# Optimization experiments

Hardware: AMD Instinct MI355X
Metric: run time of the kernel (lower is better)

Reference implementation:

```python
import jax, jax.numpy as jnp
import numpy as np

HID = 1024
BATCH = 32
SRC = 2048

def setup_inputs() -> dict:
    key = jax.random.key(0)
    k1, k2, k3, k4, k5 = jax.random.split(key, 5)
    hidden = jax.random.normal(k1, (BATCH, HID), dtype=jnp.float32)
    encoder_outputs = jax.random.normal(k2, (BATCH, SRC, HID), dtype=jnp.float32)
    # nn.Linear(2H, H): weight [H, 2H], bias [H]
    lim = 1.0 / np.sqrt(2 * HID)
    attn_w = jax.random.uniform(k3, (HID, 2 * HID), dtype=jnp.float32, minval=-lim, maxval=lim)
    attn_b = jax.random.uniform(k4, (HID,), dtype=jnp.float32, minval=-lim, maxval=lim)
    v = jax.random.uniform(k5, (HID,), dtype=jnp.float32)  # torch.rand
    return {"hidden": hidden, "encoder_outputs": encoder_outputs,
            "attn_w": attn_w, "attn_b": attn_b, "v": v}

def reference(hidden, encoder_outputs, attn_w, attn_b, v):
    # Split the concat linear: cat([hidden, enc]) @ W^T == hidden @ Wh^T + enc @ We^T
    w_h = attn_w[:, :HID]          # [H, H] acts on repeated hidden
    w_e = attn_w[:, HID:]          # [H, H] acts on encoder outputs
    # energy: [B, S, H]
    energy = jnp.tanh(
        jnp.einsum('bh,oh->bo', hidden, w_h)[:, None, :]
        + jnp.einsum('bsh,oh->bso', encoder_outputs, w_e)
        + attn_b
    )
    scores = jnp.einsum('bso,o->bs', energy, v)  # [B, S]
    return jax.nn.softmax(scores, axis=1)
```

## Files before the change

kernel.cpp:

```cpp
#include <hip/hip_runtime.h>
#include <hip/hip_bf16.h>

#define HID    1024
#define NBATCH 32
#define SRC    2048
#define MROWS  (NBATCH * SRC)

typedef _Float16 f16;
typedef f16   f16x8 __attribute__((ext_vector_type(8)));
typedef f16   f16x4 __attribute__((ext_vector_type(4)));
typedef float f32x4 __attribute__((ext_vector_type(4)));

#define BAR()    asm volatile("s_barrier" ::: "memory")
#define VMCNT0() asm volatile("s_waitcnt vmcnt(0)" ::: "memory")

__device__ __forceinline__ void gload_lds16(const void* g, void* l) {
  __builtin_amdgcn_global_load_lds(
      (const __attribute__((address_space(1))) void*)g,
      (__attribute__((address_space(3))) void*)l, 16, 0, 0);
}

__device__ __forceinline__ float fast_tanh(float x) {
  x = fminf(fmaxf(x, -15.f), 15.f);
  float e = __expf(2.f * x);
  return (e - 1.f) / (e + 1.f);
}

__global__ void convw_k(const float* __restrict__ attn_w, f16* __restrict__ Wf) {
  int idx = blockIdx.x * 256 + threadIdx.x;
  int j = idx * 4;
  int o = j >> 10, h = j & 1023;
  f32x4 d = *(const f32x4*)(attn_w + (size_t)o * 2048 + HID + h);
  f16x4 q = { (f16)d[0], (f16)d[1], (f16)d[2], (f16)d[3] };
  *(f16x4*)(Wf + (size_t)o * HID + h) = q;
}

__global__ void hvec_k(const float* __restrict__ hidden,
                       const float* __restrict__ attn_w,
                       const float* __restrict__ attn_b,
                       float* __restrict__ hvec) {
  int idx = blockIdx.x * 256 + threadIdx.x;
  int b = idx >> 10, o = idx & 1023;
  const float* wrow = attn_w + (size_t)o * 2048;
  const float* hrow = hidden + (size_t)b * HID;
  float acc = 0.f;
  for (int h = 0; h < HID; h += 4) {
    f32x4 wv = *(const f32x4*)(wrow + h);
    f32x4 hv = *(const f32x4*)(hrow + h);
    acc += wv[0]*hv[0] + wv[1]*hv[1] + wv[2]*hv[2] + wv[3]*hv[3];
  }
  hvec[idx] = acc + attn_b[o];
}

__global__ void convA_k(const float* __restrict__ A, f16* __restrict__ Af) {
  size_t i = ((size_t)blockIdx.x * 256 + threadIdx.x) * 8;
  f32x4 d0 = *(const f32x4*)(A + i);
  f32x4 d1 = *(const f32x4*)(A + i + 4);
  f16x8 q = { (f16)d0[0], (f16)d0[1], (f16)d0[2], (f16)d0[3],
              (f16)d1[0], (f16)d1[1], (f16)d1[2], (f16)d1[3] };
  *(f16x8*)(Af + i) = q;
}


#define STG1(q, Tn, cd) do { \
  const f16* s_ = ((q) < 4 ? Ab : Bb) + \
      (size_t)(((q) & 3) * 64 + (tid >> 3)) * HID + (Tn) * 64 + scol; \
  char* d_ = lds + (cd) * 65536 + ((q) < 4 ? 0 : 32768) + ((q) & 3) * 8192 + w * 1024; \
  gload_lds16(s_, d_); } while (0)

#define PHASE(P, Tn, c, DOSTG) do { \
  const int mh_ = (P) >> 1, nh_ = (P) & 1; \
  const char* la_ = lds + (c) * 65536; \
  const char* lb_ = la_ + 32768; \
  f16x8 aF[4][2], bF[2][2]; \
  _Pragma("unroll") for (int m4 = 0; m4 < 4; ++m4) { \
    const char* rb = la_ + (wr * 128 + mh_ * 64 + m4 * 16 + lr) * 128; \
    aF[m4][0] = *(const f16x8*)(rb + ((lg ^ sw) << 4)); \
    aF[m4][1] = *(const f16x8*)(rb + (((4 + lg) ^ sw) << 4)); \
  } \
  _Pragma("unroll") for (int n2 = 0; n2 < 2; ++n2) { \
    const char* rb = lb_ + (wc * 64 + nh_ * 32 + n2 * 16 + lr) * 128; \
    bF[n2][0] = *(const f16x8*)(rb + ((lg ^ sw) << 4)); \
    bF[n2][1] = *(const f16x8*)(rb + (((4 + lg) ^ sw) << 4)); \
  } \
  if (DOSTG) { STG1(2 * (P), Tn, (c) ^ 1); STG1(2 * (P) + 1, Tn, (c) ^ 1); } \
  BAR(); \
  asm volatile("s_waitcnt lgkmcnt(0)" ::: "memory"); \
  __builtin_amdgcn_sched_barrier(0); \
  __builtin_amdgcn_s_setprio(1); \
  _Pragma("unroll") for (int ks = 0; ks < 2; ++ks) \
  _Pragma("unroll") for (int m4 = 0; m4 < 4; ++m4) \
  _Pragma("unroll") for (int n2 = 0; n2 < 2; ++n2) \
    acc[mh_ * 4 + m4][nh_ * 2 + n2] = __builtin_amdgcn_mfma_f32_16x16x32_f16( \
        aF[m4][ks], bF[n2][ks], acc[mh_ * 4 + m4][nh_ * 2 + n2], 0, 0, 0); \
  __builtin_amdgcn_s_setprio(0); \
  if ((P) == 3 && (DOSTG)) { VMCNT0(); } \
  BAR(); \
} while (0)

__global__ __launch_bounds__(512, 2) void gemm_f16(
    const f16*  __restrict__ Af,
    const f16*  __restrict__ Wf,
    const float* __restrict__ hvec,
    const float* __restrict__ v,
    float* __restrict__ part)
{
  extern __shared__ __align__(16) char lds[];

  int bid = blockIdx.x;
  int wg = (bid & 7) * 128 + (bid >> 3);
  int m_idx = wg >> 2, n_idx = wg & 3;
  long row0 = (long)m_idx * 256;
  int o0 = n_idx * 256;
  int b = (int)(row0 >> 11);

  int tid = threadIdx.x;
  int l = tid & 63, w = tid >> 6;
  int wr = w >> 2, wc = w & 3;
  int lr = l & 15, lg = l >> 4;
  int sw = lr & 7;
  int scol = ((tid & 7) ^ ((tid >> 3) & 7)) * 8;

  const f16* Ab = Af + row0 * HID;
  const f16* Bb = Wf + (size_t)o0 * HID;

  f32x4 acc[8][4];
#pragma unroll
  for (int m = 0; m < 8; ++m)
#pragma unroll
    for (int n = 0; n < 4; ++n) acc[m][n] = (f32x4){0.f, 0.f, 0.f, 0.f};

#pragma unroll
  for (int q = 0; q < 8; ++q) { STG1(q, 0, 0); }
  VMCNT0(); BAR();

#pragma unroll 1
  for (int Tp = 0; Tp < 8; ++Tp) {
    const int Ta = Tp * 2, Tb = Ta + 1;
    PHASE(0, Ta + 1, 0, 1); PHASE(1, Ta + 1, 0, 1);
    PHASE(2, Ta + 1, 0, 1); PHASE(3, Ta + 1, 0, 1);
    const int dob = (Tb < 15);
    PHASE(0, Tb + 1, 1, dob); PHASE(1, Tb + 1, 1, dob);
    PHASE(2, Tb + 1, 1, dob); PHASE(3, Tb + 1, 1, dob);
  }

  float hvv[4], vvv[4];
#pragma unroll
  for (int n = 0; n < 4; ++n) {
    int o = o0 + wc * 64 + n * 16 + lr;
    hvv[n] = hvec[b * HID + o];
    vvv[n] = v[o];
  }
  float* scf = (float*)lds;
  __syncthreads();
#pragma unroll
  for (int m = 0; m < 8; ++m) {
#pragma unroll
    for (int r = 0; r < 4; ++r) {
      float s = 0.f;
#pragma unroll
      for (int n = 0; n < 4; ++n)
        s += fast_tanh(acc[m][n][r] + hvv[n]) * vvv[n];
      s += __shfl_xor(s, 1); s += __shfl_xor(s, 2);
      s += __shfl_xor(s, 4); s += __shfl_xor(s, 8);
      if (lr == 0) scf[wc * 256 + wr * 128 + m * 16 + lg * 4 + r] = s;
    }
  }
  __syncthreads();
  if (tid < 256)
    part[(size_t)n_idx * MROWS + row0 + tid] =
        scf[tid] + scf[256 + tid] + scf[512 + tid] + scf[768 + tid];
}

__global__ __launch_bounds__(256, 2) void gemm_fb(
    const float* __restrict__ A, const f16* __restrict__ Wf,
    const float* __restrict__ hvec, const float* __restrict__ v,
    float* __restrict__ part)
{
  __shared__ __align__(16) f16 lA[128][32];
  __shared__ __align__(16) f16 lB[128][32];
  __shared__ float sc[128];

  int bid = blockIdx.x;
  int x = bid & 7, j = bid >> 3;
  int m_idx = x * 64 + (j >> 3);
  int n_idx = j & 7;
  long row0 = (long)m_idx * 128;
  int o0 = n_idx * 128;
  int b = (int)(row0 >> 11);

  int tid = threadIdx.x;
  int l = tid & 63, w = tid >> 6;
  int wr = w >> 1, wc = w & 1;
  int lr = l & 15, lg = l >> 4;

  f32x4 acc[4][4];
#pragma unroll
  for (int m = 0; m < 4; ++m)
#pragma unroll
    for (int n = 0; n < 4; ++n) acc[m][n] = (f32x4){0.f, 0.f, 0.f, 0.f};

  const float* Abase = A + row0 * 1024;

  for (int k0 = 0; k0 < 1024; k0 += 32) {
    __syncthreads();
#pragma unroll
    for (int i = 0; i < 2; ++i) {
      int rr = (i * 256 + tid) >> 2;
      const f16* src = Wf + (size_t)(o0 + rr) * HID + k0 + (tid & 3) * 8;
      char* ldsb = (char*)&lB[0][0] + i * 4096 + w * 1024;
      gload_lds16(src, ldsb);
    }
#pragma unroll
    for (int i = 0; i < 4; ++i) {
      int ja = i * 256 + tid;
      int arow = ja >> 3, ac4 = ja & 7;
      f32x4 d = *(const f32x4*)(Abase + (size_t)arow * 1024 + k0 + ac4 * 4);
      f16x4 q = { (f16)d[0], (f16)d[1], (f16)d[2], (f16)d[3] };
      *(f16x4*)&lA[arow][ac4 * 4] = q;
    }
    __syncthreads();
    f16x8 aF[4], bF[4];
#pragma unroll
    for (int m = 0; m < 4; ++m)
      aF[m] = *(const f16x8*)&lA[wr * 64 + m * 16 + lr][lg * 8];
#pragma unroll
    for (int n = 0; n < 4; ++n)
      bF[n] = *(const f16x8*)&lB[wc * 64 + n * 16 + lr][lg * 8];
#pragma unroll
    for (int m = 0; m < 4; ++m)
#pragma unroll
      for (int n = 0; n < 4; ++n)
        acc[m][n] = __builtin_amdgcn_mfma_f32_16x16x32_f16(aF[m], bF[n], acc[m][n], 0, 0, 0);
  }

  float hv[4], vv[4];
#pragma unroll
  for (int n = 0; n < 4; ++n) {
    int o = o0 + wc * 64 + n * 16 + lr;
    hv[n] = hvec[b * HID + o];
    vv[n] = v[o];
  }
  float myv[4][4];
#pragma unroll
  for (int m = 0; m < 4; ++m) {
#pragma unroll
    for (int r = 0; r < 4; ++r) {
      float s = 0.f;
#pragma unroll
      for (int n = 0; n < 4; ++n)
        s += fast_tanh(acc[m][n][r] + hv[n]) * vv[n];
      s += __shfl_xor(s, 1); s += __shfl_xor(s, 2);
      s += __shfl_xor(s, 4); s += __shfl_xor(s, 8);
      myv[m][r] = s;
    }
  }
  if (wc == 0 && lr == 0) {
#pragma unroll
    for (int m = 0; m < 4; ++m)
#pragma unroll
      for (int r = 0; r < 4; ++r)
        sc[wr * 64 + m * 16 + lg * 4 + r] = myv[m][r];
  }
  __syncthreads();
  if (wc == 1 && lr == 0) {
#pragma unroll
    for (int m = 0; m < 4; ++m)
#pragma unroll
      for (int r = 0; r < 4; ++r)
        sc[wr * 64 + m * 16 + lg * 4 + r] += myv[m][r];
  }
  __syncthreads();
  if (tid < 128)
    part[(size_t)n_idx * MROWS + row0 + tid] = sc[tid];
}

__global__ void softmax_k(const float* __restrict__ part, float* __restrict__ out,
                          int nsl) {
  int b = blockIdx.x;
  __shared__ float srow[SRC];
  __shared__ float red[8];
  int tid = threadIdx.x;

  float lmax = -1e30f;
  for (int i = tid; i < SRC; i += 256) {
    float s = 0.f;
    for (int t = 0; t < nsl; ++t)
      s += part[(size_t)t * MROWS + (size_t)b * SRC + i];
    srow[i] = s;
    lmax = fmaxf(lmax, s);
  }
#pragma unroll
  for (int off = 32; off >= 1; off >>= 1)
    lmax = fmaxf(lmax, __shfl_xor(lmax, off));
  if ((tid & 63) == 0) red[tid >> 6] = lmax;
  __syncthreads();
  float bmax = fmaxf(fmaxf(red[0], red[1]), fmaxf(red[2], red[3]));

  float lsum = 0.f;
  for (int i = tid; i < SRC; i += 256) {
    float e = __expf(srow[i] - bmax);
    srow[i] = e;
    lsum += e;
  }
#pragma unroll
  for (int off = 32; off >= 1; off >>= 1)
    lsum += __shfl_xor(lsum, off);
  if ((tid & 63) == 0) red[4 + (tid >> 6)] = lsum;
  __syncthreads();
  float inv = 1.f / (red[4] + red[5] + red[6] + red[7]);
  for (int i = tid; i < SRC; i += 256)
    out[(size_t)b * SRC + i] = srow[i] * inv;
}

extern "C" void kernel_launch(void* const* d_in, const int* in_sizes, int n_in,
                              void* d_out, int out_size, void* d_ws, size_t ws_size,
                              hipStream_t stream) {
  const float* hidden = (const float*)d_in[0];
  const float* enc    = (const float*)d_in[1];
  const float* attn_w = (const float*)d_in[2];
  const float* attn_b = (const float*)d_in[3];
  const float* v      = (const float*)d_in[4];
  float* out = (float*)d_out;

  char* ws = (char*)d_ws;
  f16*   Wf   = (f16*)ws;
  float* hv   = (float*)(ws + (2ull << 20));
  float* part = (float*)(ws + (2ull << 20) + (128ull << 10));
  f16*   Af   = (f16*)(ws + (8ull << 20));

  const size_t WS_NEEDED = (8ull << 20) + (128ull << 20);

  convw_k<<<1024, 256, 0, stream>>>(attn_w, Wf);
  hvec_k <<<128,  256, 0, stream>>>(hidden, attn_w, attn_b, hv);

  if (ws_size >= WS_NEEDED) {
    convA_k<<<32768, 256, 0, stream>>>(enc, Af);
    gemm_f16<<<1024, 512, 131072, stream>>>(Af, Wf, hv, v, part);
    softmax_k<<<NBATCH, 256, 0, stream>>>(part, out, 4);
  } else {
    gemm_fb<<<4096, 256, 0, stream>>>(enc, Wf, hv, v, part);
    softmax_k<<<NBATCH, 256, 0, stream>>>(part, out, 8);
  }
}
```

Measured before the change: 300.9 us.

## Reorder GEMM phases to reuse A/B fragments across MFMA quadrants

Restructures each K-tile of the f16 GEMM from four independent phases (each reloading its A and B fragments from LDS) into a snake order that keeps A fragments and two B fragment sets in registers across quadrants. This cuts LDS fragment reads per tile and groups the global-to-LDS stages into one A burst and one B burst. It also replaces the asm barrier with the builtin and drops the memory clobbers, which loosens compiler ordering. The extra live fragment registers could raise register pressure at the 512x2 launch bound.

```diff
diff --git a/kernel.cpp b/kernel.cpp
--- a/kernel.cpp
+++ b/kernel.cpp
@@ -11,8 +11,10 @@
 typedef f16   f16x4 __attribute__((ext_vector_type(4)));
 typedef float f32x4 __attribute__((ext_vector_type(4)));
 
-#define BAR()    asm volatile("s_barrier" ::: "memory")
-#define VMCNT0() asm volatile("s_waitcnt vmcnt(0)" ::: "memory")
+#define BAR()    __builtin_amdgcn_s_barrier()
+#define LGKM0()  asm volatile("s_waitcnt lgkmcnt(0)")
+#define VMCNT0() asm volatile("s_waitcnt vmcnt(0)")
+#define SCHED0() __builtin_amdgcn_sched_barrier(0)
 
 __device__ __forceinline__ void gload_lds16(const void* g, void* l) {
   __builtin_amdgcn_global_load_lds(
@@ -62,40 +64,59 @@
 }
 
 
-#define STG1(q, Tn, cd) do { \
-  const f16* s_ = ((q) < 4 ? Ab : Bb) + \
-      (size_t)(((q) & 3) * 64 + (tid >> 3)) * HID + (Tn) * 64 + scol; \
-  char* d_ = lds + (cd) * 65536 + ((q) < 4 ? 0 : 32768) + ((q) & 3) * 8192 + w * 1024; \
-  gload_lds16(s_, d_); } while (0)
-
-#define PHASE(P, Tn, c, DOSTG) do { \
-  const int mh_ = (P) >> 1, nh_ = (P) & 1; \
-  const char* la_ = lds + (c) * 65536; \
-  const char* lb_ = la_ + 32768; \
-  f16x8 aF[4][2], bF[2][2]; \
+#define STG_A(Tn, cd) do { \
+  _Pragma("unroll") for (int q_ = 0; q_ < 4; ++q_) \
+    gload_lds16(Ab + (size_t)(q_ * 64 + (tid >> 3)) * HID + (Tn) * 64 + scol, \
+                lds + (cd) * 65536 + q_ * 8192 + w * 1024); } while (0)
+#define STG_B(Tn, cd) do { \
+  _Pragma("unroll") for (int q_ = 0; q_ < 4; ++q_) \
+    gload_lds16(Bb + (size_t)(q_ * 64 + (tid >> 3)) * HID + (Tn) * 64 + scol, \
+                lds + (cd) * 65536 + 32768 + q_ * 8192 + w * 1024); } while (0)
+
+#define RD_A(la_, mh_) do { \
   _Pragma("unroll") for (int m4 = 0; m4 < 4; ++m4) { \
-    const char* rb = la_ + (wr * 128 + mh_ * 64 + m4 * 16 + lr) * 128; \
+    const char* rb = (la_) + (wr * 128 + (mh_) * 64 + m4 * 16 + lr) * 128; \
     aF[m4][0] = *(const f16x8*)(rb + ((lg ^ sw) << 4)); \
-    aF[m4][1] = *(const f16x8*)(rb + (((4 + lg) ^ sw) << 4)); \
-  } \
+    aF[m4][1] = *(const f16x8*)(rb + (((4 + lg) ^ sw) << 4)); } } while (0)
+#define RD_B(lb_, dst, nh_) do { \
   _Pragma("unroll") for (int n2 = 0; n2 < 2; ++n2) { \
-    const char* rb = lb_ + (wc * 64 + nh_ * 32 + n2 * 16 + lr) * 128; \
-    bF[n2][0] = *(const f16x8*)(rb + ((lg ^ sw) << 4)); \
-    bF[n2][1] = *(const f16x8*)(rb + (((4 + lg) ^ sw) << 4)); \
-  } \
-  if (DOSTG) { STG1(2 * (P), Tn, (c) ^ 1); STG1(2 * (P) + 1, Tn, (c) ^ 1); } \
-  BAR(); \
-  asm volatile("s_waitcnt lgkmcnt(0)" ::: "memory"); \
-  __builtin_amdgcn_sched_barrier(0); \
+    const char* rb = (lb_) + (wc * 64 + (nh_) * 32 + n2 * 16 + lr) * 128; \
+    dst[n2][0] = *(const f16x8*)(rb + ((lg ^ sw) << 4)); \
+    dst[n2][1] = *(const f16x8*)(rb + (((4 + lg) ^ sw) << 4)); } } while (0)
+
+#define MFMA16(bsrc, mo, no) do { \
   __builtin_amdgcn_s_setprio(1); \
   _Pragma("unroll") for (int ks = 0; ks < 2; ++ks) \
   _Pragma("unroll") for (int m4 = 0; m4 < 4; ++m4) \
   _Pragma("unroll") for (int n2 = 0; n2 < 2; ++n2) \
-    acc[mh_ * 4 + m4][nh_ * 2 + n2] = __builtin_amdgcn_mfma_f32_16x16x32_f16( \
-        aF[m4][ks], bF[n2][ks], acc[mh_ * 4 + m4][nh_ * 2 + n2], 0, 0, 0); \
-  __builtin_amdgcn_s_setprio(0); \
-  if ((P) == 3 && (DOSTG)) { VMCNT0(); } \
-  BAR(); \
+    acc[(mo) + m4][(no) + n2] = __builtin_amdgcn_mfma_f32_16x16x32_f16( \
+        aF[m4][ks], bsrc[n2][ks], acc[(mo) + m4][(no) + n2], 0, 0, 0); \
+  __builtin_amdgcn_s_setprio(0); } while (0)
+
+#define TILE(c, Tn, DOSTG) do { \
+  const char* la_ = lds + (c) * 65536; \
+  const char* lb_ = la_ + 32768; \
+   \
+  RD_A(la_, 0); RD_B(lb_, bF0, 0); \
+  if (DOSTG) STG_A(Tn, (c) ^ 1); \
+  BAR(); LGKM0(); SCHED0(); \
+  MFMA16(bF0, 0, 0); \
+  BAR(); SCHED0(); \
+   \
+  RD_B(lb_, bF1, 1); \
+  if (DOSTG) STG_B(Tn, (c) ^ 1); \
+  BAR(); LGKM0(); SCHED0(); \
+  MFMA16(bF1, 0, 2); \
+  BAR(); SCHED0(); \
+   \
+  RD_A(la_, 1); \
+  BAR(); LGKM0(); SCHED0(); \
+  MFMA16(bF1, 4, 2); \
+  BAR(); SCHED0(); \
+   \
+  MFMA16(bF0, 4, 0); \
+  if (DOSTG) { VMCNT0(); SCHED0(); } \
+  BAR(); SCHED0(); \
 } while (0)
 
 __global__ __launch_bounds__(512, 2) void gemm_f16(
@@ -130,18 +151,16 @@
 #pragma unroll
     for (int n = 0; n < 4; ++n) acc[m][n] = (f32x4){0.f, 0.f, 0.f, 0.f};
 
-#pragma unroll
-  for (int q = 0; q < 8; ++q) { STG1(q, 0, 0); }
-  VMCNT0(); BAR();
+  f16x8 aF[4][2], bF0[2][2], bF1[2][2];
+
+  STG_A(0, 0); STG_B(0, 0);
+  VMCNT0(); SCHED0(); BAR(); SCHED0();
 
 #pragma unroll 1
   for (int Tp = 0; Tp < 8; ++Tp) {
     const int Ta = Tp * 2, Tb = Ta + 1;
-    PHASE(0, Ta + 1, 0, 1); PHASE(1, Ta + 1, 0, 1);
-    PHASE(2, Ta + 1, 0, 1); PHASE(3, Ta + 1, 0, 1);
-    const int dob = (Tb < 15);
-    PHASE(0, Tb + 1, 1, dob); PHASE(1, Tb + 1, 1, dob);
-    PHASE(2, Tb + 1, 1, dob); PHASE(3, Tb + 1, 1, dob);
+    TILE(0, Ta + 1, 1);
+    TILE(1, Tb + 1, (Tb < 15));
   }
 
   float hvv[4], vvv[4];
```

Result: faster. 291.7 us (-3.1%).

## Restructure f16 GEMM: 256x128 tiles, triple-buffered A in LDS, B in registers

Applied to the files above, without the earlier changes.

Narrows the GEMM output tile from 256x256 to 256x128 and doubles the grid so each output chunk yields eight partial score rows instead of four. A tiles are now triple-buffered in LDS, using 96KB instead of 128KB. Each wave loads its W fragments straight from global memory into double-buffered registers, skipping the LDS staging for B. The main loop is fully unrolled into tiles with explicit vmcnt waits, so loads overlap MFMA work with fewer barriers. The trade-off is redundant B reads served by the cache, a second A read per row band, and higher register pressure.

```diff
diff --git a/kernel.cpp b/kernel.cpp
--- a/kernel.cpp
+++ b/kernel.cpp
@@ -11,8 +11,8 @@
 typedef f16   f16x4 __attribute__((ext_vector_type(4)));
 typedef float f32x4 __attribute__((ext_vector_type(4)));
 
-#define BAR()    asm volatile("s_barrier" ::: "memory")
-#define VMCNT0() asm volatile("s_waitcnt vmcnt(0)" ::: "memory")
+#define BAR()    __builtin_amdgcn_s_barrier()
+#define SCHED0() __builtin_amdgcn_sched_barrier(0)
 
 __device__ __forceinline__ void gload_lds16(const void* g, void* l) {
   __builtin_amdgcn_global_load_lds(
@@ -62,39 +62,52 @@
 }
 
 
-#define STG1(q, Tn, cd) do { \
-  const f16* s_ = ((q) < 4 ? Ab : Bb) + \
-      (size_t)(((q) & 3) * 64 + (tid >> 3)) * HID + (Tn) * 64 + scol; \
-  char* d_ = lds + (cd) * 65536 + ((q) < 4 ? 0 : 32768) + ((q) & 3) * 8192 + w * 1024; \
-  gload_lds16(s_, d_); } while (0)
-
-#define PHASE(P, Tn, c, DOSTG) do { \
-  const int mh_ = (P) >> 1, nh_ = (P) & 1; \
-  const char* la_ = lds + (c) * 65536; \
-  const char* lb_ = la_ + 32768; \
-  f16x8 aF[4][2], bF[2][2]; \
-  _Pragma("unroll") for (int m4 = 0; m4 < 4; ++m4) { \
-    const char* rb = la_ + (wr * 128 + mh_ * 64 + m4 * 16 + lr) * 128; \
-    aF[m4][0] = *(const f16x8*)(rb + ((lg ^ sw) << 4)); \
-    aF[m4][1] = *(const f16x8*)(rb + (((4 + lg) ^ sw) << 4)); \
-  } \
-  _Pragma("unroll") for (int n2 = 0; n2 < 2; ++n2) { \
-    const char* rb = lb_ + (wc * 64 + nh_ * 32 + n2 * 16 + lr) * 128; \
-    bF[n2][0] = *(const f16x8*)(rb + ((lg ^ sw) << 4)); \
-    bF[n2][1] = *(const f16x8*)(rb + (((4 + lg) ^ sw) << 4)); \
-  } \
-  if (DOSTG) { STG1(2 * (P), Tn, (c) ^ 1); STG1(2 * (P) + 1, Tn, (c) ^ 1); } \
-  BAR(); \
-  asm volatile("s_waitcnt lgkmcnt(0)" ::: "memory"); \
-  __builtin_amdgcn_sched_barrier(0); \
+#define STG_A3(Tn, bi) do { \
+  _Pragma("unroll") for (int q_ = 0; q_ < 4; ++q_) \
+    gload_lds16(Ab + (size_t)(q_ * 64 + (tid >> 3)) * HID + (Tn) * 64 + scol, \
+                lds + (bi) * 32768 + q_ * 8192 + w * 1024); } while (0)
+
+#define RD_AF(dst, mh_, bi) do { \
+  const char* ab_ = lds + (bi) * 32768; \
+  _Pragma("unroll") for (int m2 = 0; m2 < 2; ++m2) { \
+    const char* rb_ = ab_ + (wr * 64 + (mh_) * 32 + m2 * 16 + lr) * 128; \
+    dst[m2][0] = *(const f16x8*)(rb_ + ((lg ^ sw) << 4)); \
+    dst[m2][1] = *(const f16x8*)(rb_ + (((4 + lg) ^ sw) << 4)); } } while (0)
+
+#define LD_B8(dst, Tn) do { \
+  _Pragma("unroll") for (int nq = 0; nq < 4; ++nq) { \
+    const f16* bp_ = Bb + (size_t)(wc * 64 + nq * 16 + lr) * HID + (Tn) * 64 + lg * 8; \
+    dst[nq][0] = *(const f16x8*)bp_; \
+    dst[nq][1] = *(const f16x8*)(bp_ + 32); } } while (0)
+
+#define MFMA8(af, mh_, nh_, bs) do { \
   __builtin_amdgcn_s_setprio(1); \
   _Pragma("unroll") for (int ks = 0; ks < 2; ++ks) \
-  _Pragma("unroll") for (int m4 = 0; m4 < 4; ++m4) \
+  _Pragma("unroll") for (int m2 = 0; m2 < 2; ++m2) \
   _Pragma("unroll") for (int n2 = 0; n2 < 2; ++n2) \
-    acc[mh_ * 4 + m4][nh_ * 2 + n2] = __builtin_amdgcn_mfma_f32_16x16x32_f16( \
-        aF[m4][ks], bF[n2][ks], acc[mh_ * 4 + m4][nh_ * 2 + n2], 0, 0, 0); \
-  __builtin_amdgcn_s_setprio(0); \
-  if ((P) == 3 && (DOSTG)) { VMCNT0(); } \
+    acc[(mh_)*2+m2][(nh_)*2+n2] = __builtin_amdgcn_mfma_f32_16x16x32_f16( \
+        af[m2][ks], bs[(nh_)*2+n2][ks], acc[(mh_)*2+m2][(nh_)*2+n2], 0, 0, 0); \
+  __builtin_amdgcn_s_setprio(0); } while (0)
+
+#define TILE(T_, bC, bN, DO2, DOB, DOR, VMN) do { \
+   \
+  RD_AF(aFB, 1, (T_) % 3); \
+  if (DO2) STG_A3((T_) + 2, ((T_) + 2) % 3); \
+  asm volatile("s_waitcnt vmcnt(" #VMN ")" ::: "memory"); \
+  SCHED0(); \
+  MFMA8(aFA, 0, 0, bC); \
+  BAR(); \
+   \
+  if (DOB) LD_B8(bN, (T_) + 1); \
+  SCHED0(); \
+  MFMA8(aFA, 0, 1, bC); \
+  BAR(); \
+   \
+  MFMA8(aFB, 1, 1, bC); \
+  BAR(); \
+   \
+  if (DOR) RD_AF(aFA, 0, ((T_) + 1) % 3); \
+  MFMA8(aFB, 1, 0, bC); \
   BAR(); \
 } while (0)
 
@@ -108,15 +121,15 @@
   extern __shared__ __align__(16) char lds[];
 
   int bid = blockIdx.x;
-  int wg = (bid & 7) * 128 + (bid >> 3);
-  int m_idx = wg >> 2, n_idx = wg & 3;
+  int wg = (bid & 7) * 256 + (bid >> 3);
+  int m_idx = wg >> 3, n_idx = wg & 7;
   long row0 = (long)m_idx * 256;
-  int o0 = n_idx * 256;
+  int o0 = n_idx * 128;
   int b = (int)(row0 >> 11);
 
   int tid = threadIdx.x;
   int l = tid & 63, w = tid >> 6;
-  int wr = w >> 2, wc = w & 3;
+  int wr = w >> 1, wc = w & 1;
   int lr = l & 15, lg = l >> 4;
   int sw = lr & 7;
   int scol = ((tid & 7) ^ ((tid >> 3) & 7)) * 8;
@@ -124,25 +137,39 @@
   const f16* Ab = Af + row0 * HID;
   const f16* Bb = Wf + (size_t)o0 * HID;
 
-  f32x4 acc[8][4];
-#pragma unroll
-  for (int m = 0; m < 8; ++m)
+  f32x4 acc[4][4];
+#pragma unroll
+  for (int m = 0; m < 4; ++m)
 #pragma unroll
     for (int n = 0; n < 4; ++n) acc[m][n] = (f32x4){0.f, 0.f, 0.f, 0.f};
 
-#pragma unroll
-  for (int q = 0; q < 8; ++q) { STG1(q, 0, 0); }
-  VMCNT0(); BAR();
-
-#pragma unroll 1
-  for (int Tp = 0; Tp < 8; ++Tp) {
-    const int Ta = Tp * 2, Tb = Ta + 1;
-    PHASE(0, Ta + 1, 0, 1); PHASE(1, Ta + 1, 0, 1);
-    PHASE(2, Ta + 1, 0, 1); PHASE(3, Ta + 1, 0, 1);
-    const int dob = (Tb < 15);
-    PHASE(0, Tb + 1, 1, dob); PHASE(1, Tb + 1, 1, dob);
-    PHASE(2, Tb + 1, 1, dob); PHASE(3, Tb + 1, 1, dob);
-  }
+  f16x8 aFA[2][2], aFB[2][2];
+  f16x8 bX[4][2], bY[4][2];
+
+  STG_A3(0, 0);
+  LD_B8(bX, 0);
+  STG_A3(1, 1);
+  asm volatile("s_waitcnt vmcnt(12)" ::: "memory");
+  SCHED0();
+  BAR();
+  RD_AF(aFA, 0, 0);
+
+  TILE( 0, bX, bY, 1, 1, 1, 4);
+  TILE( 1, bY, bX, 1, 1, 1, 4);
+  TILE( 2, bX, bY, 1, 1, 1, 4);
+  TILE( 3, bY, bX, 1, 1, 1, 4);
+  TILE( 4, bX, bY, 1, 1, 1, 4);
+  TILE( 5, bY, bX, 1, 1, 1, 4);
+  TILE( 6, bX, bY, 1, 1, 1, 4);
+  TILE( 7, bY, bX, 1, 1, 1, 4);
+  TILE( 8, bX, bY, 1, 1, 1, 4);
+  TILE( 9, bY, bX, 1, 1, 1, 4);
+  TILE(10, bX, bY, 1, 1, 1, 4);
+  TILE(11, bY, bX, 1, 1, 1, 4);
+  TILE(12, bX, bY, 1, 1, 1, 4);
+  TILE(13, bY, bX, 1, 1, 1, 4);
+  TILE(14, bX, bY, 0, 1, 1, 0);
+  TILE(15, bY, bX, 0, 0, 0, 0);
 
   float hvv[4], vvv[4];
 #pragma unroll
@@ -154,7 +181,7 @@
   float* scf = (float*)lds;
   __syncthreads();
 #pragma unroll
-  for (int m = 0; m < 8; ++m) {
+  for (int m = 0; m < 4; ++m) {
 #pragma unroll
     for (int r = 0; r < 4; ++r) {
       float s = 0.f;
@@ -163,13 +190,12 @@
         s += fast_tanh(acc[m][n][r] + hvv[n]) * vvv[n];
       s += __shfl_xor(s, 1); s += __shfl_xor(s, 2);
       s += __shfl_xor(s, 4); s += __shfl_xor(s, 8);
-      if (lr == 0) scf[wc * 256 + wr * 128 + m * 16 + lg * 4 + r] = s;
+      if (lr == 0) scf[wc * 256 + wr * 64 + m * 16 + lg * 4 + r] = s;
     }
   }
   __syncthreads();
   if (tid < 256)
-    part[(size_t)n_idx * MROWS + row0 + tid] =
-        scf[tid] + scf[256 + tid] + scf[512 + tid] + scf[768 + tid];
+    part[(size_t)n_idx * MROWS + row0 + tid] = scf[tid] + scf[256 + tid];
 }
 
 __global__ __launch_bounds__(256, 2) void gemm_fb(
@@ -336,8 +362,8 @@
 
   if (ws_size >= WS_NEEDED) {
     convA_k<<<32768, 256, 0, stream>>>(enc, Af);
-    gemm_f16<<<1024, 512, 131072, stream>>>(Af, Wf, hv, v, part);
-    softmax_k<<<NBATCH, 256, 0, stream>>>(part, out, 4);
+    gemm_f16<<<2048, 512, 98304, stream>>>(Af, Wf, hv, v, part);
+    softmax_k<<<NBATCH, 256, 0, stream>>>(part, out, 8);
   } else {
     gemm_fb<<<4096, 256, 0, stream>>>(enc, Wf, hv, v, part);
     softmax_k<<<NBATCH, 256, 0, stream>>>(part, out, 8);
```

Result: slower. 500.5 us (+66.3%).
